# Kernel tuning notes

Measured on AMD Instinct MI355X. Metric: run time of the kernel, lower is better.

Reference implementation:

```python
import jax, jax.numpy as jnp
import numpy as np

B, D, E, H, T = 16384, 1024, 8, 512, 256
NUM_TASKS = 3  # purchase, quality, price


def setup_inputs() -> dict:
    key = jax.random.key(0)
    ks = jax.random.split(key, 12)
    s_in = 1.0 / np.sqrt(D)
    s_h = 1.0 / np.sqrt(H)
    s_t = 1.0 / np.sqrt(T)
    return {
        "x": jax.random.normal(ks[0], (B, D), dtype=jnp.float32),
        # expert layer 1: [E, D, H], layer 2: [E, H, H]
        "We1": jax.random.uniform(ks[1], (E, D, H), jnp.float32, -s_in, s_in),
        "be1": jax.random.uniform(ks[2], (E, H), jnp.float32, -s_in, s_in),
        "We2": jax.random.uniform(ks[3], (E, H, H), jnp.float32, -s_h, s_h),
        "be2": jax.random.uniform(ks[4], (E, H), jnp.float32, -s_h, s_h),
        # gates (one per task): [T_tasks, D, E]
        "Wg": jax.random.uniform(ks[5], (NUM_TASKS, D, E), jnp.float32, -s_in, s_in),
        "bg": jax.random.uniform(ks[6], (NUM_TASKS, E), jnp.float32, -s_in, s_in),
        # towers: [T_tasks, H, T] then [T_tasks, T, 1]
        "Wt1": jax.random.uniform(ks[7], (NUM_TASKS, H, T), jnp.float32, -s_h, s_h),
        "bt1": jax.random.uniform(ks[8], (NUM_TASKS, T), jnp.float32, -s_h, s_h),
        "Wt2": jax.random.uniform(ks[9], (NUM_TASKS, T, 1), jnp.float32, -s_t, s_t),
        "bt2": jax.random.uniform(ks[10], (NUM_TASKS, 1), jnp.float32, -s_t, s_t),
    }


def reference(x, We1, be1, We2, be2, Wg, bg, Wt1, bt1, Wt2, bt2):
    # Batched expert MLPs (dropout = identity in eval): [B, E, H]
    h1 = jax.nn.relu(jnp.einsum("bd,edh->beh", x, We1) + be1)
    expert_out = jax.nn.relu(jnp.einsum("beh,ehk->bek", h1, We2) + be2)
    # Per-task softmax gates: [T, B, E]
    gates = jax.nn.softmax(jnp.einsum("bd,tde->tbe", x, Wg) + bg[:, None, :], axis=-1)
    # Weighted combine: [T, B, H]
    task_in = jnp.einsum("tbe,beh->tbh", gates, expert_out)
    # Towers: [T, B, 1]
    th = jax.nn.relu(jnp.einsum("tbh,thk->tbk", task_in, Wt1) + bt1[:, None, :])
    preds = jax.nn.sigmoid(jnp.einsum("tbk,tko->tbo", th, Wt2) + bt2[:, None, :])
    return (preds[0], preds[1], preds[2])
```

## Files before the change

kernel.cpp:

```cpp
#include <hip/hip_runtime.h>


#define BM 128
#define BN 128
#define BK 64

typedef __attribute__((ext_vector_type(8))) short short8;
typedef __attribute__((ext_vector_type(4))) float floatx4;
typedef __attribute__((ext_vector_type(4))) unsigned short ushortx4;
typedef __attribute__((ext_vector_type(8))) unsigned short ushortx8;

__device__ __forceinline__ unsigned short f32_to_bf16(float f) {
  unsigned int u = __float_as_uint(f);
  u += 0x7fffu + ((u >> 16) & 1u);
  return (unsigned short)(u >> 16);
}
__device__ __forceinline__ float bf16_to_f32(unsigned short h) {
  return __uint_as_float(((unsigned int)h) << 16);
}

__device__ __forceinline__ void async_cp16(const void* g, void* lds) {
  __builtin_amdgcn_global_load_lds(
      (const __attribute__((address_space(1))) void*)g,
      (__attribute__((address_space(3))) void*)lds, 16, 0, 0);
}

__device__ __forceinline__ void transpose_slice(
    const float* __restrict__ in, unsigned short* __restrict__ out,
    int K, int N, float (*tile)[33]) {
  int n0 = blockIdx.x * 32, k0 = blockIdx.y * 32;
  for (int i = threadIdx.y; i < 32; i += 8)
    tile[i][threadIdx.x] = in[(size_t)(k0 + i) * N + n0 + threadIdx.x];
  __syncthreads();
  for (int i = threadIdx.y; i < 32; i += 8)
    out[(size_t)(n0 + i) * K + k0 + threadIdx.x] = f32_to_bf16(tile[threadIdx.x][i]);
}

__global__ void prep_kernel(const float* __restrict__ We1, const float* __restrict__ We2,
                            const float* __restrict__ Wt1, const float* __restrict__ Wg,
                            unsigned short* __restrict__ W1T, unsigned short* __restrict__ W2T,
                            unsigned short* __restrict__ Wt1T, float* __restrict__ WgT) {
  __shared__ float tile[32][33];
  int z = blockIdx.z;
  if (z < 8) {
    transpose_slice(We1 + (size_t)z * 524288, W1T + (size_t)z * 524288, 1024, 512, tile);
  } else if (z < 16) {
    if (blockIdx.y < 16)
      transpose_slice(We2 + (size_t)(z - 8) * 262144, W2T + (size_t)(z - 8) * 262144, 512, 512, tile);
  } else if (z < 19) {
    if (blockIdx.x < 8 && blockIdx.y < 16)
      transpose_slice(Wt1 + (size_t)(z - 16) * 131072, Wt1T + (size_t)(z - 16) * 131072, 512, 256, tile);
  } else {
    if (blockIdx.x < 16 && blockIdx.y < 6) {
      int idx = (blockIdx.y * 16 + blockIdx.x) * 256 + threadIdx.y * 32 + threadIdx.x;
      int t = idx >> 13, r = idx & 8191, e = r >> 10, d = r & 1023;
      WgT[idx] = Wg[t * 8192 + d * 8 + e];
    }
  }
}

__global__ __launch_bounds__(256) void gates_cvt_kernel(
    const float* __restrict__ x, const float* __restrict__ WgT,
    const float* __restrict__ bg, float* __restrict__ gout,
    unsigned short* __restrict__ xb) {
  int wave = threadIdx.x >> 6, lane = threadIdx.x & 63;
  int b = blockIdx.x * 4 + wave;
  const float* xr = x + (size_t)b * 1024;
  float xv[16];
#pragma unroll
  for (int j = 0; j < 16; j++) xv[j] = xr[lane + 64 * j];
  unsigned short* xbr = xb + (size_t)b * 1024;
#pragma unroll
  for (int j = 0; j < 16; j++) xbr[lane + 64 * j] = f32_to_bf16(xv[j]);
  float mylogit = 0.f;
#pragma unroll
  for (int te = 0; te < 24; te++) {
    const float* w = WgT + te * 1024;
    float a = 0.f;
#pragma unroll
    for (int j = 0; j < 16; j++) a += xv[j] * w[lane + 64 * j];
#pragma unroll
    for (int off = 32; off > 0; off >>= 1) a += __shfl_xor(a, off, 64);
    if (lane == te) mylogit = a;
  }
  if (lane < 24) {
    int t = lane >> 3, e = lane & 7;
    float logit = mylogit + bg[lane];
    float m = logit;
    m = fmaxf(m, __shfl_xor(m, 4, 64));
    m = fmaxf(m, __shfl_xor(m, 2, 64));
    m = fmaxf(m, __shfl_xor(m, 1, 64));
    float ex = __expf(logit - m);
    float s = ex;
    s += __shfl_xor(s, 4, 64);
    s += __shfl_xor(s, 2, 64);
    s += __shfl_xor(s, 1, 64);
    gout[(size_t)t * 131072 + (size_t)b * 8 + e] = ex / s;
  }
}

__global__ __launch_bounds__(256) void gemm_bt_relu(
    const unsigned short* __restrict__ Abase, long aOffZ, int lda,
    const unsigned short* __restrict__ Bbase, long bOffZ,
    const float* __restrict__ biasBase, int biasOffZ,
    unsigned short* __restrict__ Cbase, long cOffZ, int ldc,
    int K) {
  __shared__ __align__(16) unsigned short As[BM * BK];
  __shared__ __align__(16) unsigned short Bs[BN * BK];
  const int tid = threadIdx.x;
  const int z = blockIdx.z;
  const unsigned short* A = Abase + (size_t)aOffZ * z + (size_t)blockIdx.x * BM * lda;
  const unsigned short* Bt = Bbase + (size_t)bOffZ * z + (size_t)blockIdx.y * BN * K;
  const float* bias = biasBase + (size_t)biasOffZ * z + blockIdx.y * BN;
  unsigned short* C = Cbase + (size_t)cOffZ * z + (size_t)blockIdx.x * BM * ldc + blockIdx.y * BN;

  const int wave = tid >> 6, lane = tid & 63;
  const int wm = (wave >> 1) * 64, wn = (wave & 1) * 64;
  const int lm = lane & 15, lq = lane >> 4;
  const int sw = lm & 7;

  floatx4 acc[4][4] = {};

  const int sr = tid >> 3;
  const int sc = (((tid & 7) ^ (sr & 7)) << 3);

  for (int kt = 0; kt < K; kt += BK) {
#pragma unroll
    for (int i = 0; i < 4; i++)
      async_cp16(A + (size_t)(sr + 32 * i) * lda + kt + sc,
                 (char*)As + i * 4096 + tid * 16);
#pragma unroll
    for (int i = 0; i < 4; i++)
      async_cp16(Bt + (size_t)(sr + 32 * i) * K + kt + sc,
                 (char*)Bs + i * 4096 + tid * 16);
    __syncthreads();
#pragma unroll
    for (int ks = 0; ks < 2; ks++) {
      short8 af[4], bf[4];
      const int ch = ((ks * 4 + lq) ^ sw) << 3;
#pragma unroll
      for (int i = 0; i < 4; i++)
        af[i] = *(const short8*)(As + (wm + 16 * i + lm) * BK + ch);
#pragma unroll
      for (int j = 0; j < 4; j++)
        bf[j] = *(const short8*)(Bs + (wn + 16 * j + lm) * BK + ch);
#pragma unroll
      for (int i = 0; i < 4; i++)
#pragma unroll
        for (int j = 0; j < 4; j++)
          acc[i][j] = __builtin_amdgcn_mfma_f32_16x16x32_bf16(af[i], bf[j], acc[i][j], 0, 0, 0);
    }
    __syncthreads();
  }

#pragma unroll
  for (int i = 0; i < 4; i++) {
    const int row = wm + 16 * i + lq * 4;
#pragma unroll
    for (int j = 0; j < 4; j++) {
      const int col = wn + 16 * j + lm;
      const float bv = bias[col];
#pragma unroll
      for (int v = 0; v < 4; v++) {
        float val = fmaxf(acc[i][j][v] + bv, 0.0f);
        C[(size_t)(row + v) * ldc + col] = f32_to_bf16(val);
      }
    }
  }
}

__global__ __launch_bounds__(256, 2) void tower_fused_kernel(
    const unsigned short* __restrict__ eoc, const float* __restrict__ gates,
    const unsigned short* __restrict__ Wt1T,
    const float* __restrict__ bt1, const float* __restrict__ Wt2,
    const float* __restrict__ bt2, float* __restrict__ out,
    int b0, int Bc) {
  __shared__ __align__(16) unsigned short As[64 * 64];
  __shared__ __align__(16) unsigned short Bs[2][256 * 64];
  const int tid = threadIdx.x;
  const int mtiles = Bc >> 6;
  const int t = blockIdx.x / mtiles;
  const int xbl = blockIdx.x % mtiles;
  const unsigned short* Bt = Wt1T + (size_t)t * 131072;

  const int wave = tid >> 6, lane = tid & 63;
  const int wn = wave * 64;
  const int lm = lane & 15, lq = lane >> 4;
  const int sw = lm & 7;
  const int sr = tid >> 3;
  const int sc = (((tid & 7) ^ (sr & 7)) << 3);

  floatx4 acc[4][4] = {};

  float gv[2][8];
#pragma unroll
  for (int r = 0; r < 2; r++) {
    const floatx4* gp = (const floatx4*)(
        gates + ((size_t)t * 16384 + b0 + (size_t)xbl * 64 + sr + 32 * r) * 8);
    floatx4 g0 = gp[0], g1 = gp[1];
#pragma unroll
    for (int j = 0; j < 4; j++) { gv[r][j] = g0[j]; gv[r][4 + j] = g1[j]; }
  }

  const unsigned short* eb0 = eoc + ((size_t)(xbl * 64 + sr) * 8) * 512 + sc;
  const unsigned short* eb1 = eoc + ((size_t)(xbl * 64 + sr + 32) * 8) * 512 + sc;

  ushortx8 pv[2][8];

#define STAGE_B_T(buf, kt_) do {                                             \
    _Pragma("unroll") for (int i_ = 0; i_ < 8; ++i_)                         \
      async_cp16(Bt + (size_t)(sr + 32 * i_) * 512 + (kt_) + sc,             \
                 (char*)Bs[buf] + i_ * 4096 + tid * 16); } while (0)

#define LOAD_PV(kt_) do {                                                    \
    _Pragma("unroll") for (int e_ = 0; e_ < 8; ++e_) {                       \
      pv[0][e_] = *(const ushortx8*)(eb0 + (size_t)e_ * 512 + (kt_));        \
      pv[1][e_] = *(const ushortx8*)(eb1 + (size_t)e_ * 512 + (kt_));        \
    } } while (0)

  STAGE_B_T(0, 0);
  LOAD_PV(0);

  for (int kt = 0; kt < 512; kt += 64) {
    const int cur = (kt >> 6) & 1;
#pragma unroll
    for (int r = 0; r < 2; r++) {
      float s[8] = {};
#pragma unroll
      for (int e = 0; e < 8; e++) {
        const float g = gv[r][e];
#pragma unroll
        for (int j = 0; j < 8; j++) s[j] += g * bf16_to_f32(pv[r][e][j]);
      }
      ushortx8 o;
#pragma unroll
      for (int j = 0; j < 8; j++) o[j] = f32_to_bf16(s[j]);
      *(ushortx8*)((char*)As + r * 4096 + tid * 16) = o;
    }
    __syncthreads();
    if (kt < 448) {
      STAGE_B_T(cur ^ 1, kt + 64);
      LOAD_PV(kt + 64);
    }
#pragma unroll
    for (int ks = 0; ks < 2; ks++) {
      short8 af[4], bf[4];
      const int ch = ((ks * 4 + lq) ^ sw) << 3;
#pragma unroll
      for (int i = 0; i < 4; i++)
        af[i] = *(const short8*)(As + (16 * i + lm) * 64 + ch);
#pragma unroll
      for (int j = 0; j < 4; j++)
        bf[j] = *(const short8*)(Bs[cur] + (wn + 16 * j + lm) * 64 + ch);
#pragma unroll
      for (int i = 0; i < 4; i++)
#pragma unroll
        for (int j = 0; j < 4; j++)
          acc[i][j] = __builtin_amdgcn_mfma_f32_16x16x32_bf16(af[i], bf[j], acc[i][j], 0, 0, 0);
    }
    __builtin_amdgcn_sched_barrier(0);
    __builtin_amdgcn_s_barrier();
    __builtin_amdgcn_sched_barrier(0);
  }

  float b1v[4], w2v[4];
#pragma unroll
  for (int j = 0; j < 4; j++) {
    int col = wn + 16 * j + lm;
    b1v[j] = bt1[t * 256 + col];
    w2v[j] = Wt2[t * 256 + col];
  }
  float* pt = (float*)As;
#pragma unroll
  for (int i = 0; i < 4; i++) {
#pragma unroll
    for (int v = 0; v < 4; v++) {
      float p = 0.f;
#pragma unroll
      for (int j = 0; j < 4; j++)
        p += fmaxf(acc[i][j][v] + b1v[j], 0.0f) * w2v[j];
      p += __shfl_xor(p, 1, 64);
      p += __shfl_xor(p, 2, 64);
      p += __shfl_xor(p, 4, 64);
      p += __shfl_xor(p, 8, 64);
      if (lm == 0) pt[(16 * i + lq * 4 + v) * 4 + wave] = p;
    }
  }
  __syncthreads();
  if (tid < 64) {
    float s = pt[tid * 4] + pt[tid * 4 + 1] + pt[tid * 4 + 2] + pt[tid * 4 + 3] + bt2[t];
    out[(t << 14) + b0 + xbl * 64 + tid] = 1.f / (1.f + __expf(-s));
  }
}

extern "C" void kernel_launch(void* const* d_in, const int* in_sizes, int n_in,
                              void* d_out, int out_size, void* d_ws, size_t ws_size,
                              hipStream_t stream) {
  (void)in_sizes; (void)n_in; (void)out_size;
  const float* x   = (const float*)d_in[0];
  const float* We1 = (const float*)d_in[1];
  const float* be1 = (const float*)d_in[2];
  const float* We2 = (const float*)d_in[3];
  const float* be2 = (const float*)d_in[4];
  const float* Wg  = (const float*)d_in[5];
  const float* bg  = (const float*)d_in[6];
  const float* Wt1 = (const float*)d_in[7];
  const float* bt1 = (const float*)d_in[8];
  const float* Wt2 = (const float*)d_in[9];
  const float* bt2 = (const float*)d_in[10];
  float* out = (float*)d_out;

  char* ws = (char*)d_ws;
  unsigned short* xb   = (unsigned short*)(ws + 0);
  unsigned short* W1T  = (unsigned short*)(ws + 33554432);
  unsigned short* W2T  = (unsigned short*)(ws + 41943040);
  unsigned short* Wt1T = (unsigned short*)(ws + 46137344);
  float*          gts  = (float*)(ws + 46923776);
  float*          WgT  = (float*)(ws + 48496640);
  const size_t fixed = 48594944;

  size_t rem = ws_size > fixed ? ws_size - fixed : 0;
  int Bc = 16384;
  while (Bc > 512 && (size_t)Bc * 16384 > rem) Bc >>= 1;
  const int nc = 16384 / Bc;

  char* cb = ws + fixed;
  unsigned short* h1c = (unsigned short*)(cb);
  unsigned short* eoc = (unsigned short*)(cb + (size_t)Bc * 8192);

  prep_kernel<<<dim3(16, 32, 20), dim3(32, 8), 0, stream>>>(We1, We2, Wt1, Wg, W1T, W2T, Wt1T, WgT);
  gates_cvt_kernel<<<4096, 256, 0, stream>>>(x, WgT, bg, gts, xb);

  for (int c = 0; c < nc; c++) {
    const unsigned short* xbc = xb + (size_t)c * Bc * 1024;
    gemm_bt_relu<<<dim3(Bc / 128, 4, 8), 256, 0, stream>>>(
        xbc, 0L, 1024, W1T, 524288L, be1, 512, h1c, 512L, 4096, 1024);
    gemm_bt_relu<<<dim3(Bc / 128, 4, 8), 256, 0, stream>>>(
        h1c, 512L, 4096, W2T, 262144L, be2, 512, eoc, 512L, 4096, 512);
    tower_fused_kernel<<<3 * (Bc / 64), 256, 0, stream>>>(
        eoc, gts, Wt1T, bt1, Wt2, bt2, out, c * Bc, Bc);
  }
}
```

Before: 484.9 us.

## Double-buffer gated combine tile and overlap it with tower MFMA loop

Double-buffers the A tile in LDS so the gate-weighted expert combine for the next K slice is computed after the current slice's MFMAs, instead of before them behind a barrier. Loads are reordered so per-thread expert loads are issued before the async LDS copies, and explicit vmcnt waits replace the second __syncthreads per iteration. The goal is to hide global-load latency and remove one barrier per iteration. The cost is more LDS, which may lower occupancy. Correctness now depends on hand-counted vmcnt values and on a redundant prefetch in the last iteration.

```diff
diff --git a/kernel.cpp b/kernel.cpp
--- a/kernel.cpp
+++ b/kernel.cpp
@@ -175,7 +175,7 @@
     const float* __restrict__ bt1, const float* __restrict__ Wt2,
     const float* __restrict__ bt2, float* __restrict__ out,
     int b0, int Bc) {
-  __shared__ __align__(16) unsigned short As[64 * 64];
+  __shared__ __align__(16) unsigned short As[2][64 * 64];
   __shared__ __align__(16) unsigned short Bs[2][256 * 64];
   const int tid = threadIdx.x;
   const int mtiles = Bc >> 6;
@@ -218,37 +218,49 @@
       pv[1][e_] = *(const ushortx8*)(eb1 + (size_t)e_ * 512 + (kt_));        \
     } } while (0)
 
+#define COMBINE_TO(buf) do {                                                 \
+    _Pragma("unroll") for (int r_ = 0; r_ < 2; ++r_) {                       \
+      float s_[8] = {};                                                      \
+      _Pragma("unroll") for (int e_ = 0; e_ < 8; ++e_) {                     \
+        const float g_ = gv[r_][e_];                                         \
+        _Pragma("unroll") for (int j_ = 0; j_ < 8; ++j_)                     \
+          s_[j_] += g_ * bf16_to_f32(pv[r_][e_][j_]);                        \
+      }                                                                      \
+      ushortx8 o_;                                                           \
+      _Pragma("unroll") for (int j_ = 0; j_ < 8; ++j_)                       \
+        o_[j_] = f32_to_bf16(s_[j_]);                                        \
+      *(ushortx8*)((char*)As[buf] + r_ * 4096 + tid * 16) = o_;              \
+    } } while (0)
+
+#define SB __builtin_amdgcn_sched_barrier(0)
+
+  LOAD_PV(0);
+  SB;
   STAGE_B_T(0, 0);
-  LOAD_PV(0);
-
-  for (int kt = 0; kt < 512; kt += 64) {
-    const int cur = (kt >> 6) & 1;
-#pragma unroll
-    for (int r = 0; r < 2; r++) {
-      float s[8] = {};
-#pragma unroll
-      for (int e = 0; e < 8; e++) {
-        const float g = gv[r][e];
-#pragma unroll
-        for (int j = 0; j < 8; j++) s[j] += g * bf16_to_f32(pv[r][e][j]);
-      }
-      ushortx8 o;
-#pragma unroll
-      for (int j = 0; j < 8; j++) o[j] = f32_to_bf16(s[j]);
-      *(ushortx8*)((char*)As + r * 4096 + tid * 16) = o;
-    }
-    __syncthreads();
-    if (kt < 448) {
-      STAGE_B_T(cur ^ 1, kt + 64);
-      LOAD_PV(kt + 64);
-    }
+  SB;
+  asm volatile("s_waitcnt vmcnt(8)" ::: "memory");
+  SB;
+  COMBINE_TO(0);
+  asm volatile("s_waitcnt lgkmcnt(0)" ::: "memory");
+  SB;
+
+  for (int k = 0; k < 8; ++k) {
+    const int cur = k & 1;
+    __builtin_amdgcn_s_barrier();
+    const int ktn = (k < 7) ? (k + 1) * 64 : 448;
+    LOAD_PV(ktn);
+    SB;
+    STAGE_B_T(cur ^ 1, ktn);
+    SB;
+    asm volatile("s_waitcnt vmcnt(24)" ::: "memory");
+    SB;
 #pragma unroll
     for (int ks = 0; ks < 2; ks++) {
       short8 af[4], bf[4];
       const int ch = ((ks * 4 + lq) ^ sw) << 3;
 #pragma unroll
       for (int i = 0; i < 4; i++)
-        af[i] = *(const short8*)(As + (16 * i + lm) * 64 + ch);
+        af[i] = *(const short8*)(As[cur] + (16 * i + lm) * 64 + ch);
 #pragma unroll
       for (int j = 0; j < 4; j++)
         bf[j] = *(const short8*)(Bs[cur] + (wn + 16 * j + lm) * 64 + ch);
@@ -258,10 +270,16 @@
         for (int j = 0; j < 4; j++)
           acc[i][j] = __builtin_amdgcn_mfma_f32_16x16x32_bf16(af[i], bf[j], acc[i][j], 0, 0, 0);
     }
-    __builtin_amdgcn_sched_barrier(0);
-    __builtin_amdgcn_s_barrier();
-    __builtin_amdgcn_sched_barrier(0);
-  }
+    if (k < 7) {
+      asm volatile("s_waitcnt vmcnt(8)" ::: "memory");
+      SB;
+      COMBINE_TO(cur ^ 1);
+      asm volatile("s_waitcnt lgkmcnt(0)" ::: "memory");
+      SB;
+    }
+  }
+
+  asm volatile("s_waitcnt vmcnt(0)" ::: "memory");
 
   float b1v[4], w2v[4];
 #pragma unroll
@@ -270,7 +288,7 @@
     b1v[j] = bt1[t * 256 + col];
     w2v[j] = Wt2[t * 256 + col];
   }
-  float* pt = (float*)As;
+  float* pt = (float*)As[0];
 #pragma unroll
   for (int i = 0; i < 4; i++) {
 #pragma unroll
```

New measurement: 505.3 us. +4.2%, slower.

## Overlap tower stage with next chunk's first expert GEMM in one launch

Applied to the files above, without the earlier changes.

Adds a combined kernel whose first blocks run the gated-combine plus tower computation for the current batch chunk. Its remaining blocks run the layer-1 expert GEMM for the next chunk. The first expert GEMM is hoisted out of the chunk loop, so later chunks get their h1 from this combined launch. The aim is to fill the GPU with both kinds of work and cut per-chunk launch and tail idle time. This only matters when the workspace forces more than one chunk; with a single chunk the launch sequence is unchanged.

```diff
diff --git a/kernel.cpp b/kernel.cpp
--- a/kernel.cpp
+++ b/kernel.cpp
@@ -293,6 +293,179 @@
   }
 }
 
+__global__ __launch_bounds__(256) void tower_gemm1_kernel(
+    const unsigned short* __restrict__ eoc, const float* __restrict__ gates,
+    const unsigned short* __restrict__ Wt1T,
+    const float* __restrict__ bt1, const float* __restrict__ Wt2,
+    const float* __restrict__ bt2, float* __restrict__ out,
+    int b0, int Bc,
+    const unsigned short* __restrict__ xbn, const unsigned short* __restrict__ W1T,
+    const float* __restrict__ be1, unsigned short* __restrict__ h1c) {
+  __shared__ __align__(16) unsigned short shmem[20480];
+  const int tid = threadIdx.x;
+  const int TB = 3 * (Bc >> 6);
+  const int wave = tid >> 6, lane = tid & 63;
+  const int lm = lane & 15, lq = lane >> 4;
+  const int sw = lm & 7;
+  const int sr = tid >> 3;
+  const int sc = (((tid & 7) ^ (sr & 7)) << 3);
+
+  if ((int)blockIdx.x < TB) {
+    unsigned short* Ast = shmem;
+    unsigned short* Bst = shmem + 4096;
+    const int mtiles = Bc >> 6;
+    const int t = blockIdx.x / mtiles;
+    const int xbl = blockIdx.x % mtiles;
+    const unsigned short* Bt = Wt1T + (size_t)t * 131072;
+    const int wn = wave * 64;
+
+    floatx4 acc[4][4] = {};
+
+    float gv[2][8];
+#pragma unroll
+    for (int r = 0; r < 2; r++) {
+      const floatx4* gp = (const floatx4*)(
+          gates + ((size_t)t * 16384 + b0 + (size_t)xbl * 64 + sr + 32 * r) * 8);
+      floatx4 g0 = gp[0], g1 = gp[1];
+#pragma unroll
+      for (int j = 0; j < 4; j++) { gv[r][j] = g0[j]; gv[r][4 + j] = g1[j]; }
+    }
+
+    const unsigned short* eb0 = eoc + ((size_t)(xbl * 64 + sr) * 8) * 512 + sc;
+    const unsigned short* eb1 = eoc + ((size_t)(xbl * 64 + sr + 32) * 8) * 512 + sc;
+
+    for (int kt = 0; kt < 512; kt += 64) {
+#pragma unroll
+      for (int i_ = 0; i_ < 8; ++i_)
+        async_cp16(Bt + (size_t)(sr + 32 * i_) * 512 + kt + sc,
+                   (char*)Bst + i_ * 4096 + tid * 16);
+#pragma unroll
+      for (int r = 0; r < 2; r++) {
+        const unsigned short* eb = r ? eb1 : eb0;
+        float s[8] = {};
+#pragma unroll
+        for (int e = 0; e < 8; e++) {
+          ushortx8 v = *(const ushortx8*)(eb + (size_t)e * 512 + kt);
+          const float g = gv[r][e];
+#pragma unroll
+          for (int j = 0; j < 8; j++) s[j] += g * bf16_to_f32(v[j]);
+        }
+        ushortx8 o;
+#pragma unroll
+        for (int j = 0; j < 8; j++) o[j] = f32_to_bf16(s[j]);
+        *(ushortx8*)((char*)Ast + r * 4096 + tid * 16) = o;
+      }
+      __syncthreads();
+#pragma unroll
+      for (int ks = 0; ks < 2; ks++) {
+        short8 af[4], bf[4];
+        const int ch = ((ks * 4 + lq) ^ sw) << 3;
+#pragma unroll
+        for (int i = 0; i < 4; i++)
+          af[i] = *(const short8*)(Ast + (16 * i + lm) * 64 + ch);
+#pragma unroll
+        for (int j = 0; j < 4; j++)
+          bf[j] = *(const short8*)(Bst + (wn + 16 * j + lm) * 64 + ch);
+#pragma unroll
+        for (int i = 0; i < 4; i++)
+#pragma unroll
+          for (int j = 0; j < 4; j++)
+            acc[i][j] = __builtin_amdgcn_mfma_f32_16x16x32_bf16(af[i], bf[j], acc[i][j], 0, 0, 0);
+      }
+      __syncthreads();
+    }
+
+    float b1v[4], w2v[4];
+#pragma unroll
+    for (int j = 0; j < 4; j++) {
+      int col = wn + 16 * j + lm;
+      b1v[j] = bt1[t * 256 + col];
+      w2v[j] = Wt2[t * 256 + col];
+    }
+    float* pt = (float*)Ast;
+#pragma unroll
+    for (int i = 0; i < 4; i++) {
+#pragma unroll
+      for (int v = 0; v < 4; v++) {
+        float p = 0.f;
+#pragma unroll
+        for (int j = 0; j < 4; j++)
+          p += fmaxf(acc[i][j][v] + b1v[j], 0.0f) * w2v[j];
+        p += __shfl_xor(p, 1, 64);
+        p += __shfl_xor(p, 2, 64);
+        p += __shfl_xor(p, 4, 64);
+        p += __shfl_xor(p, 8, 64);
+        if (lm == 0) pt[(16 * i + lq * 4 + v) * 4 + wave] = p;
+      }
+    }
+    __syncthreads();
+    if (tid < 64) {
+      float s = pt[tid * 4] + pt[tid * 4 + 1] + pt[tid * 4 + 2] + pt[tid * 4 + 3] + bt2[t];
+      out[(t << 14) + b0 + xbl * 64 + tid] = 1.f / (1.f + __expf(-s));
+    }
+  } else {
+    unsigned short* As = shmem;
+    unsigned short* Bs = shmem + 8192;
+    const int rb = blockIdx.x - TB;
+    const int nbx = Bc >> 7;
+    const int bx = rb % nbx;
+    const int by = (rb / nbx) & 3;
+    const int bz = rb / (nbx * 4);
+    const unsigned short* A = xbn + (size_t)bx * BM * 1024;
+    const unsigned short* Bt = W1T + (size_t)bz * 524288 + (size_t)by * BN * 1024;
+    const float* bias = be1 + bz * 512 + by * BN;
+    unsigned short* C = h1c + (size_t)bx * BM * 4096 + bz * 512 + by * BN;
+
+    const int wm = (wave >> 1) * 64, wn = (wave & 1) * 64;
+
+    floatx4 acc[4][4] = {};
+
+    for (int kt = 0; kt < 1024; kt += BK) {
+#pragma unroll
+      for (int i = 0; i < 4; i++)
+        async_cp16(A + (size_t)(sr + 32 * i) * 1024 + kt + sc,
+                   (char*)As + i * 4096 + tid * 16);
+#pragma unroll
+      for (int i = 0; i < 4; i++)
+        async_cp16(Bt + (size_t)(sr + 32 * i) * 1024 + kt + sc,
+                   (char*)Bs + i * 4096 + tid * 16);
+      __syncthreads();
+#pragma unroll
+      for (int ks = 0; ks < 2; ks++) {
+        short8 af[4], bf[4];
+        const int ch = ((ks * 4 + lq) ^ sw) << 3;
+#pragma unroll
+        for (int i = 0; i < 4; i++)
+          af[i] = *(const short8*)(As + (wm + 16 * i + lm) * BK + ch);
+#pragma unroll
+        for (int j = 0; j < 4; j++)
+          bf[j] = *(const short8*)(Bs + (wn + 16 * j + lm) * BK + ch);
+#pragma unroll
+        for (int i = 0; i < 4; i++)
+#pragma unroll
+          for (int j = 0; j < 4; j++)
+            acc[i][j] = __builtin_amdgcn_mfma_f32_16x16x32_bf16(af[i], bf[j], acc[i][j], 0, 0, 0);
+      }
+      __syncthreads();
+    }
+
+#pragma unroll
+    for (int i = 0; i < 4; i++) {
+      const int row = wm + 16 * i + lq * 4;
+#pragma unroll
+      for (int j = 0; j < 4; j++) {
+        const int col = wn + 16 * j + lm;
+        const float bv = bias[col];
+#pragma unroll
+        for (int v = 0; v < 4; v++) {
+          float val = fmaxf(acc[i][j][v] + bv, 0.0f);
+          C[(size_t)(row + v) * 4096 + col] = f32_to_bf16(val);
+        }
+      }
+    }
+  }
+}
+
 extern "C" void kernel_launch(void* const* d_in, const int* in_sizes, int n_in,
                               void* d_out, int out_size, void* d_ws, size_t ws_size,
                               hipStream_t stream) {
@@ -331,13 +504,20 @@
   prep_kernel<<<dim3(16, 32, 20), dim3(32, 8), 0, stream>>>(We1, We2, Wt1, Wg, W1T, W2T, Wt1T, WgT);
   gates_cvt_kernel<<<4096, 256, 0, stream>>>(x, WgT, bg, gts, xb);
 
+  gemm_bt_relu<<<dim3(Bc / 128, 4, 8), 256, 0, stream>>>(
+      xb, 0L, 1024, W1T, 524288L, be1, 512, h1c, 512L, 4096, 1024);
   for (int c = 0; c < nc; c++) {
-    const unsigned short* xbc = xb + (size_t)c * Bc * 1024;
-    gemm_bt_relu<<<dim3(Bc / 128, 4, 8), 256, 0, stream>>>(
-        xbc, 0L, 1024, W1T, 524288L, be1, 512, h1c, 512L, 4096, 1024);
     gemm_bt_relu<<<dim3(Bc / 128, 4, 8), 256, 0, stream>>>(
         h1c, 512L, 4096, W2T, 262144L, be2, 512, eoc, 512L, 4096, 512);
-    tower_fused_kernel<<<3 * (Bc / 64), 256, 0, stream>>>(
-        eoc, gts, Wt1T, bt1, Wt2, bt2, out, c * Bc, Bc);
-  }
-}
+    if (c < nc - 1) {
+      const unsigned short* xbn = xb + (size_t)(c + 1) * Bc * 1024;
+      const int TB = 3 * (Bc >> 6);
+      const int GB = (Bc >> 7) * 32;
+      tower_gemm1_kernel<<<TB + GB, 256, 0, stream>>>(
+          eoc, gts, Wt1T, bt1, Wt2, bt2, out, c * Bc, Bc, xbn, W1T, be1, h1c);
+    } else {
+      tower_fused_kernel<<<3 * (Bc / 64), 256, 0, stream>>>(
+          eoc, gts, Wt1T, bt1, Wt2, bt2, out, c * Bc, Bc);
+    }
+  }
+}
```

After: 507.6 us. +4.7%, slower.
